# Kernel optimization log

Measured on AMD Instinct MI355X. Metric: run time of the kernel, lower is better.

## Reference

```python
import jax, jax.numpy as jnp
import numpy as np

N = 8192
TEMP = 0.5
EPS = 1e-12


def _normalize(z):
    # F.normalize(z, p=2, dim=1): x / max(||x||, eps)
    n = jnp.sqrt(jnp.sum(z * z, axis=1, keepdims=True))
    return z / jnp.maximum(n, EPS)


def _gcn(edge_index, edge_weight, x, w, b):
    # torch.sparse.mm(adj, x @ w): out[row] += adj[row, col] * support[col]
    support = x @ w
    msg = support[edge_index[1]] * edge_weight[:, None]
    return jax.ops.segment_sum(msg, edge_index[0], num_segments=N) + b


def _encoder(edge_index, edge_weight, feat, w_l1a, b_l1a, w_l1b, b_l1b, w_g1, b_g1, w_g2, b_g2):
    x = jax.nn.relu(feat @ w_l1a + b_l1a) @ w_l1b + b_l1b  # [N, 32]
    h = jax.nn.relu(_gcn(edge_index, edge_weight, x, w_g1, b_g1))  # [N, hid]
    return _gcn(edge_index, edge_weight, h, w_g2, b_g2)  # [N, act_fn]


def _proj(h, w_fc1, b_fc1, w_fc2, b_fc2):
    return jax.nn.elu(h @ w_fc1 + b_fc1) @ w_fc2 + b_fc2


def _loss(z1, z2):
    z1n = _normalize(z1)
    z2n = _normalize(z2)
    refl = jnp.exp((z1n @ z1n.T) / TEMP)      # [N, N]
    between = jnp.exp((z1n @ z2n.T) / TEMP)   # [N, N]
    denom = refl.sum(1) + between.sum(1) - jnp.diagonal(refl)
    return -jnp.log(jnp.diagonal(between) / denom)


def setup_inputs() -> dict:
    key = jax.random.key(0)
    ks = jax.random.split(key, 20)
    E = 262144
    in_dim, hid_dim, act_fn, out_dim = 512, 256, 128, 64

    def kaiming(k, shape):
        fan_in = shape[0]
        bound = np.sqrt(6.0 / fan_in)
        return jax.random.uniform(k, shape, jnp.float32, -bound, bound)

    return {
        "feat1": jax.random.normal(ks[0], (N, in_dim), jnp.float32),
        "feat2": jax.random.normal(ks[1], (N, in_dim), jnp.float32),
        "edge_index1": jax.random.randint(ks[2], (2, E), 0, N, jnp.int32),
        "edge_weight1": jax.random.uniform(ks[3], (E,), jnp.float32),
        "edge_index2": jax.random.randint(ks[4], (2, E), 0, N, jnp.int32),
        "edge_weight2": jax.random.uniform(ks[5], (E,), jnp.float32),
        "w_l1a": kaiming(ks[6], (in_dim, 64)),
        "b_l1a": jnp.zeros((64,), jnp.float32),
        "w_l1b": kaiming(ks[7], (64, 32)),
        "b_l1b": jnp.zeros((32,), jnp.float32),
        "w_g1": kaiming(ks[8], (32, hid_dim)),
        "b_g1": jnp.zeros((hid_dim,), jnp.float32),
        "w_g2": kaiming(ks[9], (hid_dim, act_fn)),
        "b_g2": jnp.zeros((act_fn,), jnp.float32),
        "w_fc1": kaiming(ks[10], (act_fn, out_dim)),
        "b_fc1": jnp.zeros((out_dim,), jnp.float32),
        "w_fc2": kaiming(ks[11], (out_dim, act_fn)),
        "b_fc2": jnp.zeros((act_fn,), jnp.float32),
    }


def reference(feat1, feat2, edge_index1, edge_weight1, edge_index2, edge_weight2,
              w_l1a, b_l1a, w_l1b, b_l1b, w_g1, b_g1, w_g2, b_g2,
              w_fc1, b_fc1, w_fc2, b_fc2):
    h1 = _encoder(edge_index1, edge_weight1, feat1, w_l1a, b_l1a, w_l1b, b_l1b, w_g1, b_g1, w_g2, b_g2)
    h2 = _encoder(edge_index2, edge_weight2, feat2, w_l1a, b_l1a, w_l1b, b_l1b, w_g1, b_g1, w_g2, b_g2)
    z1 = _proj(h1, w_fc1, b_fc1, w_fc2, b_fc2)
    z2 = _proj(h2, w_fc1, b_fc1, w_fc2, b_fc2)
    l1 = _loss(z1, z2)
    l2 = _loss(z2, z1)
    return ((l1 + l2) * 0.5).mean()
```

## Files before the change

### kernel.cpp

```cpp
#include <hip/hip_runtime.h>
#include <hip/hip_bf16.h>
#include <math.h>


#define NROWS 8192
#define MROWS 16384
#define NEDGE 262144

typedef __attribute__((ext_vector_type(8))) short bf16x8;
typedef __attribute__((ext_vector_type(4))) float f32x4;
typedef __attribute__((ext_vector_type(2))) float f32x2;
typedef long long i64;

__device__ __forceinline__ short f2bf(float f){
  union { float f; unsigned u; } cv; cv.f = f;
  unsigned u = cv.u;
  unsigned r = (u + 0x7fffu + ((u >> 16) & 1u)) >> 16;
  return (short)r;
}
__device__ __forceinline__ f32x4 mfma16(bf16x8 a, bf16x8 b, f32x4 c){
  return __builtin_amdgcn_mfma_f32_16x16x32_bf16(a, b, c, 0, 0, 0);
}
__device__ __forceinline__ float fexp2(float x){
#if __has_builtin(__builtin_amdgcn_exp2f)
  return __builtin_amdgcn_exp2f(x);
#else
  return exp2f(x);
#endif
}

__device__ unsigned char f2e4m3_sw(float f){
  float a = fabsf(f);
  unsigned s = (__float_as_uint(f)>>24)&0x80u;
  if (!(a>0.f)) return (unsigned char)s;
  if (a>448.f) a=448.f;
  int e; frexpf(a,&e);
  int eff=e-1;
  unsigned code;
  if (eff<-6){
    float q=rintf(a*512.f);
    code=(unsigned)q; if(code>7)code=7;
  } else {
    float q=rintf(a*exp2f((float)(3-eff)));
    unsigned mant=(unsigned)q;
    if(mant>=16){mant=8;eff++;}
    if(eff>8) return (unsigned char)(s|0x7e);
    code=((unsigned)(eff+7)<<3)|(mant-8);
  }
  return (unsigned char)(s|code);
}
__device__ __forceinline__ unsigned short pack2fp8(float a, float b){
#if __has_builtin(__builtin_amdgcn_cvt_pk_fp8_f32)
  int v = __builtin_amdgcn_cvt_pk_fp8_f32(a, b, 0, false);
  return (unsigned short)(v & 0xffff);
#else
  return (unsigned short)((unsigned)f2e4m3_sw(a) | ((unsigned)f2e4m3_sw(b)<<8));
#endif
}

struct WtArgs {
  const float* src[6];
  short* dst[6];
  int K[6], N[6];
  int off[7];
  int nwt;
};
__global__ void setup_k(WtArgs a, const int* __restrict__ ei1, const int* __restrict__ ei2,
                        int* __restrict__ deg1, int* __restrict__ deg2){
  int b = blockIdx.x;
  if (b < a.nwt){
    int i = b*256 + threadIdx.x;
    if (i >= a.off[6]) return;
    int s = 0;
    #pragma unroll
    for (int j=1;j<6;j++) if (i >= a.off[j]) s=j;
    int l = i - a.off[s];
    int K=a.K[s], N=a.N[s];
    int k=l/N, n=l-k*N;
    a.dst[s][(long)n*K+k] = f2bf(a.src[s][l]);
  } else {
    int hb = b - a.nwt;
    const int* ei = (hb < NEDGE/256) ? ei1 : ei2;
    int* deg = (hb < NEDGE/256) ? deg1 : deg2;
    int e = (hb % (NEDGE/256))*256 + threadIdx.x;
    atomicAdd(&deg[ei[e]], 1);
  }
}

__global__ __launch_bounds__(256) void mlp12_k(const float* __restrict__ F0, const float* __restrict__ F1,
                                               const short* __restrict__ Wa, const float* __restrict__ ba,
                                               const short* __restrict__ Wb, const float* __restrict__ bb,
                                               short* __restrict__ xb){
  __shared__ short As[32*520];
  __shared__ short a1s[32*72];
  const int tid = threadIdx.x;
  const int m0 = blockIdx.x*32;
  const float* F = (m0 < NROWS) ? (F0 + (long)m0*512) : (F1 + (long)(m0-NROWS)*512);
  {
    float4 st[16];
    #pragma unroll
    for (int i=0;i<16;i++) st[i] = *(const float4*)(F + (long)(i*256+tid)*4);
    #pragma unroll
    for (int i=0;i<16;i++){
      int idx = i*256+tid, row = idx>>7, c4 = idx&127;
      unsigned lo = (unsigned)(unsigned short)f2bf(st[i].x) | ((unsigned)(unsigned short)f2bf(st[i].y)<<16);
      unsigned hi = (unsigned)(unsigned short)f2bf(st[i].z) | ((unsigned)(unsigned short)f2bf(st[i].w)<<16);
      uint2 o = {lo, hi};
      *(uint2*)&As[row*520 + c4*4] = o;
    }
  }
  __syncthreads();
  const int wave = tid>>6, lane = tid&63, quad = lane>>4, cl = lane&15;
  f32x4 zero = {0.f,0.f,0.f,0.f};
  {
    const int wno = wave*16;
    f32x4 acc[2] = {zero, zero};
    #pragma unroll
    for (int kc=0;kc<16;kc++){
      const int ko = kc*32 + quad*8;
      bf16x8 a0 = *(const bf16x8*)&As[(cl)*520 + ko];
      bf16x8 a1 = *(const bf16x8*)&As[(16+cl)*520 + ko];
      bf16x8 b = *(const bf16x8*)(Wa + (long)(wno + cl)*512 + ko);
      acc[0] = mfma16(a0, b, acc[0]);
      acc[1] = mfma16(a1, b, acc[1]);
    }
    int col = wno + cl;
    float bv = ba[col];
    #pragma unroll
    for (int mt=0;mt<2;mt++)
      #pragma unroll
      for (int r=0;r<4;r++)
        a1s[(mt*16 + quad*4 + r)*72 + col] = f2bf(fmaxf(acc[mt][r] + bv, 0.f));
  }
  __syncthreads();
  if (wave < 2){
    f32x4 acc2[2] = {zero, zero};
    #pragma unroll
    for (int kc=0;kc<2;kc++){
      const int ko = kc*32 + quad*8;
      bf16x8 a = *(const bf16x8*)&a1s[(wave*16+cl)*72 + ko];
      #pragma unroll
      for (int nt=0;nt<2;nt++){
        bf16x8 b = *(const bf16x8*)(Wb + (long)(nt*16 + cl)*64 + ko);
        acc2[nt] = mfma16(a, b, acc2[nt]);
      }
    }
    #pragma unroll
    for (int nt=0;nt<2;nt++){
      int col = nt*16 + cl;
      float bv = bb[col];
      #pragma unroll
      for (int r=0;r<4;r++)
        xb[(long)(m0 + wave*16 + quad*4 + r)*32 + col] = f2bf(acc2[nt][r] + bv);
    }
  }
}

__global__ void scan2_k(const int* __restrict__ deg1, int* __restrict__ rs1, int* __restrict__ cur1,
                        const int* __restrict__ deg2, int* __restrict__ rs2, int* __restrict__ cur2){
  const int* deg = blockIdx.x ? deg2 : deg1;
  int* rowstart = blockIdx.x ? rs2 : rs1;
  int* cursor = blockIdx.x ? cur2 : cur1;
  __shared__ int csum[256];
  __shared__ int base[257];
  int t = threadIdx.x;
  int loc[32];
  int s = 0;
  for (int j=0;j<32;j++){ int d = deg[t*32+j]; loc[j] = s; s += d; }
  csum[t] = s;
  __syncthreads();
  if (t==0){ int a=0; for (int i=0;i<256;i++){ base[i]=a; a+=csum[i]; } base[256]=a; }
  __syncthreads();
  for (int j=0;j<32;j++){ int v = base[t] + loc[j]; rowstart[t*32+j]=v; cursor[t*32+j]=v; }
  if (t==0) rowstart[NROWS] = base[256];
}
__global__ void fill2_k(const int* __restrict__ ei1, const float* __restrict__ w1, int* __restrict__ cur1,
                        int* __restrict__ ecol1, float* __restrict__ ew1,
                        const int* __restrict__ ei2, const float* __restrict__ w2, int* __restrict__ cur2,
                        int* __restrict__ ecol2, float* __restrict__ ew2){
  int b = blockIdx.x;
  bool g2 = (b >= NEDGE/256);
  const int* ei = g2 ? ei2 : ei1;
  const float* w = g2 ? w2 : w1;
  int* cursor = g2 ? cur2 : cur1;
  int* ecol = g2 ? ecol2 : ecol1;
  float* ew = g2 ? ew2 : ew1;
  int e = (b % (NEDGE/256))*256 + threadIdx.x;
  int r = ei[e];
  int p = atomicAdd(&cursor[r], 1);
  ecol[p] = ei[NEDGE + e];
  ew[p] = w[e];
}

__device__ __forceinline__ void acc8(float* acc, int4 v, float f){
  const unsigned* u = (const unsigned*)&v;
  #pragma unroll
  for (int i=0;i<4;i++){
    union{unsigned x; float y;} lo, hi;
    lo.x = u[i] << 16;
    hi.x = u[i] & 0xffff0000u;
    acc[2*i]   = fmaf(f, lo.y, acc[2*i]);
    acc[2*i+1] = fmaf(f, hi.y, acc[2*i+1]);
  }
}
template<int C>
__device__ __forceinline__ void gather_row(float* acc, const short* sb,
                                           const int* ec, const float* w, int s, int e){
  int k = s;
  for (; k+16 <= e; k+=16){
    int c[16]; float f[16]; int4 v[16];
    #pragma unroll
    for (int u=0;u<16;u++){ c[u]=ec[k+u]; f[u]=w[k+u]; }
    #pragma unroll
    for (int u=0;u<16;u++) v[u] = *(const int4*)(sb + (long)c[u]*C);
    #pragma unroll
    for (int u=0;u<16;u++) acc8(acc, v[u], f[u]);
  }
  for (; k+4 <= e; k+=4){
    int c0=ec[k],c1=ec[k+1],c2=ec[k+2],c3=ec[k+3];
    float f0=w[k],f1=w[k+1],f2=w[k+2],f3=w[k+3];
    int4 v0 = *(const int4*)(sb + (long)c0*C);
    int4 v1 = *(const int4*)(sb + (long)c1*C);
    int4 v2 = *(const int4*)(sb + (long)c2*C);
    int4 v3 = *(const int4*)(sb + (long)c3*C);
    acc8(acc,v0,f0); acc8(acc,v1,f1); acc8(acc,v2,f2); acc8(acc,v3,f3);
  }
  for (; k < e; k++){
    int4 v0 = *(const int4*)(sb + (long)ec[k]*C);
    acc8(acc,v0,w[k]);
  }
}

template<int C, bool RELU, bool HASB>
__global__ __launch_bounds__(256) void gather_k(const short* __restrict__ sup,
    const int* __restrict__ rs1, const int* __restrict__ ec1, const float* __restrict__ w1,
    const int* __restrict__ rs2, const int* __restrict__ ec2, const float* __restrict__ w2,
    const float* __restrict__ bias, short* __restrict__ out){
  constexpr int G = C/8;
  const int g = threadIdx.x % G;
  const int sub = threadIdx.x / G;
  const int row = blockIdx.x*(256/G) + sub;
  const int* rs; const int* ec; const float* w; int soff, lr;
  if (row < NROWS){ rs=rs1; ec=ec1; w=w1; soff=0; lr=row; }
  else            { rs=rs2; ec=ec2; w=w2; soff=NROWS; lr=row-NROWS; }
  const short* sb = sup + (long)soff*C + g*8;
  float acc[8];
  #pragma unroll
  for (int j=0;j<8;j++) acc[j] = HASB ? bias[g*8+j] : 0.f;
  gather_row<C>(acc, sb, ec, w, rs[lr], rs[lr+1]);
  int4 ov;
  unsigned* ou = (unsigned*)&ov;
  #pragma unroll
  for (int i=0;i<4;i++){
    float a0 = acc[2*i], a1 = acc[2*i+1];
    if (RELU){ a0 = fmaxf(a0,0.f); a1 = fmaxf(a1,0.f); }
    ou[i] = (unsigned)(unsigned short)f2bf(a0) | ((unsigned)(unsigned short)f2bf(a1)<<16);
  }
  *(int4*)(out + (long)row*C + g*8) = ov;
}

__global__ __launch_bounds__(256) void gg_k(const short* __restrict__ xb,
    const int* __restrict__ rs1, const int* __restrict__ ec1, const float* __restrict__ w1,
    const int* __restrict__ rs2, const int* __restrict__ ec2, const float* __restrict__ w2,
    const short* __restrict__ Wg1, const float* __restrict__ bg1,
    const short* __restrict__ Wg2, short* __restrict__ s2){
  __shared__ short axs[64*40];
  __shared__ short hbs[64*264];
  const int tid = threadIdx.x;
  const int m0 = blockIdx.x*64;
  {
    const int g = tid & 3, sub = tid >> 2;
    const int row = m0 + sub;
    const int* rs; const int* ec; const float* w; int soff, lr;
    if (row < NROWS){ rs=rs1; ec=ec1; w=w1; soff=0; lr=row; }
    else            { rs=rs2; ec=ec2; w=w2; soff=NROWS; lr=row-NROWS; }
    const short* sb = xb + (long)soff*32 + g*8;
    float acc[8];
    #pragma unroll
    for (int j=0;j<8;j++) acc[j] = 0.f;
    gather_row<32>(acc, sb, ec, w, rs[lr], rs[lr+1]);
    int4 ov;
    unsigned* ou = (unsigned*)&ov;
    #pragma unroll
    for (int i=0;i<4;i++)
      ou[i] = (unsigned)(unsigned short)f2bf(acc[2*i]) | ((unsigned)(unsigned short)f2bf(acc[2*i+1])<<16);
    *(int4*)&axs[sub*40 + g*8] = ov;
  }
  __syncthreads();
  const int wave = tid>>6, lane = tid&63, quad = lane>>4, cl = lane&15;
  f32x4 zero = {0.f,0.f,0.f,0.f};
  {
    const int wno = wave*64;
    f32x4 acc[4][4];
    #pragma unroll
    for (int i=0;i<4;i++)
      #pragma unroll
      for (int j=0;j<4;j++) acc[i][j]=zero;
    const int ko = quad*8;
    bf16x8 a[4], b[4];
    #pragma unroll
    for (int mt=0;mt<4;mt++)
      a[mt] = *(const bf16x8*)&axs[(mt*16+cl)*40 + ko];
    #pragma unroll
    for (int nt=0;nt<4;nt++)
      b[nt] = *(const bf16x8*)(Wg1 + (long)(wno + nt*16 + cl)*32 + ko);
    #pragma unroll
    for (int mt=0;mt<4;mt++)
      #pragma unroll
      for (int nt=0;nt<4;nt++)
        acc[mt][nt] = mfma16(a[mt], b[nt], acc[mt][nt]);
    #pragma unroll
    for (int nt=0;nt<4;nt++){
      int col = wno + nt*16 + cl;
      float bv = bg1[col];
      #pragma unroll
      for (int mt=0;mt<4;mt++)
        #pragma unroll
        for (int r=0;r<4;r++)
          hbs[(mt*16 + quad*4 + r)*264 + col] = f2bf(fmaxf(acc[mt][nt][r] + bv, 0.f));
    }
  }
  __syncthreads();
  {
    const int wno = wave*32;
    f32x4 acc[4][2];
    #pragma unroll
    for (int i=0;i<4;i++){ acc[i][0]=zero; acc[i][1]=zero; }
    #pragma unroll
    for (int kc=0;kc<8;kc++){
      const int ko = kc*32 + quad*8;
      bf16x8 a[4], b[2];
      #pragma unroll
      for (int mt=0;mt<4;mt++)
        a[mt] = *(const bf16x8*)&hbs[(mt*16+cl)*264 + ko];
      #pragma unroll
      for (int nt=0;nt<2;nt++)
        b[nt] = *(const bf16x8*)(Wg2 + (long)(wno + nt*16 + cl)*256 + ko);
      #pragma unroll
      for (int mt=0;mt<4;mt++)
        #pragma unroll
        for (int nt=0;nt<2;nt++)
          acc[mt][nt] = mfma16(a[mt], b[nt], acc[mt][nt]);
    }
    #pragma unroll
    for (int mt=0;mt<4;mt++)
      #pragma unroll
      for (int nt=0;nt<2;nt++){
        int col = wno + nt*16 + cl;
        #pragma unroll
        for (int r=0;r<4;r++)
          s2[(long)(m0 + mt*16 + quad*4 + r)*128 + col] = f2bf(acc[mt][nt][r]);
      }
  }
}

__global__ __launch_bounds__(256) void pn_k(const short* __restrict__ hh,
    const short* __restrict__ Wf1, const float* __restrict__ bf1,
    const short* __restrict__ Wf2, const float* __restrict__ bf2,
    unsigned short* __restrict__ Zf, float* __restrict__ bdot){
  __shared__ short hs[64*136];
  __shared__ short t2s[64*72];
  __shared__ float zs[64*132];
  __shared__ float sp[4][64];
  __shared__ float dp[4][32];
  __shared__ float rnS[64];
  const float SQKE = 1.6986436f;
  const int tid = threadIdx.x;
  const int wave = tid>>6, lane = tid&63, quad = lane>>4, cl = lane&15;
  const int m0h = blockIdx.x*32;
  {
    const short* r1 = hh + (long)m0h*128;
    const short* r2 = hh + (long)(NROWS + m0h)*128;
    #pragma unroll
    for (int i=0;i<2;i++){
      int idx = i*256 + tid;
      int row = idx >> 4, c16 = idx & 15;
      *(int4*)&hs[row*136 + c16*8] = *(const int4*)(r1 + row*128 + c16*8);
      *(int4*)&hs[(32+row)*136 + c16*8] = *(const int4*)(r2 + row*128 + c16*8);
    }
  }
  __syncthreads();
  f32x4 zero = {0.f,0.f,0.f,0.f};
  {
    const int wno = wave*16;
    f32x4 acc[4];
    #pragma unroll
    for (int i=0;i<4;i++) acc[i]=zero;
    #pragma unroll
    for (int kc=0;kc<4;kc++){
      const int ko = kc*32 + quad*8;
      bf16x8 a[4], b;
      #pragma unroll
      for (int mt=0;mt<4;mt++)
        a[mt] = *(const bf16x8*)&hs[(mt*16+cl)*136 + ko];
      b = *(const bf16x8*)(Wf1 + (long)(wno + cl)*128 + ko);
      #pragma unroll
      for (int mt=0;mt<4;mt++) acc[mt] = mfma16(a[mt], b, acc[mt]);
    }
    int col = wno + cl;
    float bv = bf1[col];
    #pragma unroll
    for (int mt=0;mt<4;mt++)
      #pragma unroll
      for (int r=0;r<4;r++){
        float v = acc[mt][r] + bv;
        v = (v > 0.f) ? v : expm1f(v);
        t2s[(mt*16 + quad*4 + r)*72 + col] = f2bf(v);
      }
  }
  __syncthreads();
  {
    const int wno = wave*32;
    f32x4 acc[4][2];
    #pragma unroll
    for (int i=0;i<4;i++){ acc[i][0]=zero; acc[i][1]=zero; }
    #pragma unroll
    for (int kc=0;kc<2;kc++){
      const int ko = kc*32 + quad*8;
      bf16x8 a[4], b[2];
      #pragma unroll
      for (int mt=0;mt<4;mt++)
        a[mt] = *(const bf16x8*)&t2s[(mt*16+cl)*72 + ko];
      #pragma unroll
      for (int nt=0;nt<2;nt++)
        b[nt] = *(const bf16x8*)(Wf2 + (long)(wno + nt*16 + cl)*64 + ko);
      #pragma unroll
      for (int mt=0;mt<4;mt++)
        #pragma unroll
        for (int nt=0;nt<2;nt++)
          acc[mt][nt] = mfma16(a[mt], b[nt], acc[mt][nt]);
    }
    #pragma unroll
    for (int mt=0;mt<4;mt++)
      #pragma unroll
      for (int nt=0;nt<2;nt++){
        int col = wno + nt*16 + cl;
        float bv = bf2[col];
        #pragma unroll
        for (int r=0;r<4;r++)
          zs[(mt*16 + quad*4 + r)*132 + col] = acc[mt][nt][r] + bv;
      }
  }
  __syncthreads();
  {
    int row = tid & 63, qtr = tid >> 6;
    const float* zr = &zs[row*132 + qtr*32];
    float s = 0.f;
    #pragma unroll 8
    for (int c=0;c<32;c++) s += zr[c]*zr[c];
    sp[qtr][row] = s;
    if (row < 32){
      const float* zb_ = &zs[(row+32)*132 + qtr*32];
      float d = 0.f;
      #pragma unroll 8
      for (int c=0;c<32;c++) d += zr[c]*zb_[c];
      dp[qtr][row] = d;
    }
  }
  __syncthreads();
  if (tid < 64){
    float ssq = sp[0][tid]+sp[1][tid]+sp[2][tid]+sp[3][tid];
    rnS[tid] = 1.f / fmaxf(sqrtf(ssq), 1e-12f);
  }
  __syncthreads();
  if (tid < 32){
    float dot = dp[0][tid]+dp[1][tid]+dp[2][tid]+dp[3][tid];
    bdot[m0h + tid] = dot * rnS[tid] * rnS[tid+32];
  }
  {
    int lr = tid >> 2;
    int grow = (lr < 32) ? (m0h + lr) : (NROWS + m0h + lr - 32);
    float s = rnS[lr] * SQKE;
    int p0 = (tid & 3)*16;
    #pragma unroll
    for (int pp=0;pp<16;pp++){
      int p = p0 + pp;
      int d = p>>1, h = p&1, kc = d>>3, q = (d>>1)&3, j4 = d&1;
      long o = ((long)(grow>>4)*512 + kc*128 + j4 + ((grow&15)+16*q)*2)*2 + h;
      Zf[o] = pack2fp8(zs[lr*132 + 2*p]*s, zs[lr*132 + 2*p + 1]*s);
    }
  }
}

__global__ __launch_bounds__(256,4) void gram3_k(const unsigned char* __restrict__ Zf,
                                                 float* __restrict__ P){
  __shared__ float srow[4][64];
  __shared__ float scol[4][64];
  const int wave = threadIdx.x>>6, lane = threadIdx.x&63;
  const int t = blockIdx.x*4 + wave;
  int ti = (int)((513.0f - sqrtf(513.0f*513.0f - 8.0f*(float)t))*0.5f);
  while ((ti+1)*256 - ((ti+1)*ti)/2 <= t) ti++;
  while (ti*256 - (ti*(ti-1))/2 > t) ti--;
  const int tj = ti + (t - (ti*256 - (ti*(ti-1))/2));
  const unsigned char* za = Zf + (long)ti*16*512 + lane*8;
  const unsigned char* zb = Zf + (long)tj*16*512 + lane*8;

  f32x4 zero = {0.f,0.f,0.f,0.f};
  f32x4 acc[4][4];
  #pragma unroll
  for (int i=0;i<4;i++)
    #pragma unroll
    for (int j=0;j<4;j++) acc[i][j]=zero;

  i64 aA[4], bA[4], aB[4], bB[4];
  #pragma unroll
  for (int x=0;x<4;x++){
    aA[x] = *(const i64*)(za + (x*4+0)*512);
    bA[x] = *(const i64*)(zb + (x*4+0)*512);
  }
  #pragma unroll
  for (int kc=0;kc<4;kc++){
    i64* ac = (kc&1) ? aB : aA;
    i64* bc = (kc&1) ? bB : bA;
    i64* an = (kc&1) ? aA : aB;
    i64* bn = (kc&1) ? bA : bB;
    if (kc<3){
      #pragma unroll
      for (int x=0;x<4;x++){
        an[x] = *(const i64*)(za + (x*4+kc+1)*512);
        bn[x] = *(const i64*)(zb + (x*4+kc+1)*512);
      }
    }
    #pragma unroll
    for (int mt=0;mt<4;mt++)
      #pragma unroll
      for (int nt=0;nt<4;nt++)
        acc[mt][nt] = __builtin_amdgcn_mfma_f32_16x16x32_fp8_fp8(ac[mt], bc[nt], acc[mt][nt], 0, 0, 0);
  }

  const int quad = lane>>4, cl = lane&15;
  f32x2 z2 = {0.f,0.f};
  f32x2 rs01[4] = {z2,z2,z2,z2}, rs23[4] = {z2,z2,z2,z2};
  f32x2 cs[4] = {z2,z2,z2,z2};
  #pragma unroll
  for (int mt=0;mt<4;mt++){
    #pragma unroll
    for (int nt=0;nt<4;nt++){
      f32x4 v = acc[mt][nt];
      float e0 = fexp2(v[0]), e1 = fexp2(v[1]);
      float e2 = fexp2(v[2]), e3 = fexp2(v[3]);
      f32x2 p01 = {e0,e1}, p23 = {e2,e3};
      rs01[mt] += p01; rs23[mt] += p23;
      cs[nt] += p01; cs[nt] += p23;
    }
  }
  #pragma unroll
  for (int mt=0;mt<4;mt++){
    union{f32x2 v; double d;} u0, u1;
    u0.v = rs01[mt]; u1.v = rs23[mt];
    #pragma unroll
    for (int m=1;m<16;m<<=1){
      union{double d; f32x2 v;} o0, o1;
      o0.d = __shfl_xor(u0.d, m); o1.d = __shfl_xor(u1.d, m);
      u0.v += o0.v; u1.v += o1.v;
    }
    if (cl==0){
      f32x4 rv = {u0.v.x, u0.v.y, u1.v.x, u1.v.y};
      *(f32x4*)&srow[wave][mt*16 + quad*4] = rv;
    }
  }
  __threadfence_block();
  P[((long)ti*256 + tj)*64 + lane] = srow[wave][lane];
  if (ti != tj){
    #pragma unroll
    for (int nt=0;nt<4;nt++){
      float s = cs[nt].x + cs[nt].y;
      s += __shfl_xor(s,16); s += __shfl_xor(s,32);
      if (quad==0) scol[wave][nt*16 + cl] = s;
    }
    __threadfence_block();
    P[((long)tj*256 + ti)*64 + lane] = scol[wave][lane];
  }
}

__global__ void rloss_k(const float* __restrict__ P, const float* __restrict__ bdot,
                        float* __restrict__ out){
  __shared__ float red[256];
  const float E2 = 7.3890560989306495f;
  int t = threadIdx.x;
  int i = blockIdx.x*256 + t;
  int j = i + NROWS;
  const float* p1 = P + (long)(i>>6)*256*64 + (i&63);
  const float* p2 = P + (long)(j>>6)*256*64 + (j&63);
  float s1 = 0.f, s2 = 0.f;
  #pragma unroll 8
  for (int b=0;b<256;b++){ s1 += p1[b*64]; s2 += p2[b*64]; }
  float lb = 2.f * bdot[i];
  float term = 0.5f * ((logf(s1 - E2) - lb) + (logf(s2 - E2) - lb));
  red[t]=term; __syncthreads();
  for (int st=128; st>0; st>>=1){ if (t<st) red[t]+=red[t+st]; __syncthreads(); }
  if (t==0) atomicAdd(out, red[0] / (float)NROWS);
}

extern "C" void kernel_launch(void* const* d_in, const int* in_sizes, int n_in,
                              void* d_out, int out_size, void* d_ws, size_t ws_size,
                              hipStream_t stream){
  const float* feat1 = (const float*)d_in[0];
  const float* feat2 = (const float*)d_in[1];
  const int*   ei1   = (const int*)d_in[2];
  const float* w1    = (const float*)d_in[3];
  const int*   ei2   = (const int*)d_in[4];
  const float* w2    = (const float*)d_in[5];
  const float* w_l1a = (const float*)d_in[6];
  const float* b_l1a = (const float*)d_in[7];
  const float* w_l1b = (const float*)d_in[8];
  const float* b_l1b = (const float*)d_in[9];
  const float* w_g1  = (const float*)d_in[10];
  const float* b_g1  = (const float*)d_in[11];
  const float* w_g2  = (const float*)d_in[12];
  const float* b_g2  = (const float*)d_in[13];
  const float* w_fc1 = (const float*)d_in[14];
  const float* b_fc1 = (const float*)d_in[15];
  const float* w_fc2 = (const float*)d_in[16];
  const float* b_fc2 = (const float*)d_in[17];

  float* P = (float*)d_ws;
  char* base = (char*)d_ws;
  size_t off = (size_t)17<<20;
  auto alloc = [&](size_t bytes)->void*{
    void* r = base + off;
    off = (off + bytes + 255) & ~(size_t)255;
    return r;
  };
  short* xb   = (short*)alloc((size_t)MROWS*32*2);
  short* s2   = (short*)alloc((size_t)MROWS*128*2);
  short* hh   = (short*)alloc((size_t)MROWS*128*2);
  short* wl1a_t = (short*)alloc(512*64*2);
  short* wl1b_t = (short*)alloc(64*32*2);
  short* wg1_t  = (short*)alloc(32*256*2);
  short* wg2_t  = (short*)alloc(256*128*2);
  short* wfc1_t = (short*)alloc(128*64*2);
  short* wfc2_t = (short*)alloc(64*128*2);
  unsigned short* Zf = (unsigned short*)alloc((size_t)MROWS*128);
  int*   deg1 = (int*)alloc(NROWS*4);
  int*   deg2 = (int*)alloc(NROWS*4);
  int* rs1  = (int*)alloc((NROWS+1)*4);
  int* cur1 = (int*)alloc(NROWS*4);
  int* rs2  = (int*)alloc((NROWS+1)*4);
  int* cur2 = (int*)alloc(NROWS*4);
  int*   ecol1 = (int*)alloc((size_t)NEDGE*4);
  float* ewt1  = (float*)alloc((size_t)NEDGE*4);
  int*   ecol2 = (int*)alloc((size_t)NEDGE*4);
  float* ewt2  = (float*)alloc((size_t)NEDGE*4);
  float* bdot  = (float*)alloc(NROWS*4);

  hipMemsetAsync(deg1, 0, (size_t)2*NROWS*4, stream);
  hipMemsetAsync(d_out, 0, sizeof(float), stream);

  WtArgs wa;
  wa.src[0]=w_l1a; wa.dst[0]=wl1a_t; wa.K[0]=512; wa.N[0]=64;
  wa.src[1]=w_l1b; wa.dst[1]=wl1b_t; wa.K[1]=64;  wa.N[1]=32;
  wa.src[2]=w_g1;  wa.dst[2]=wg1_t;  wa.K[2]=32;  wa.N[2]=256;
  wa.src[3]=w_g2;  wa.dst[3]=wg2_t;  wa.K[3]=256; wa.N[3]=128;
  wa.src[4]=w_fc1; wa.dst[4]=wfc1_t; wa.K[4]=128; wa.N[4]=64;
  wa.src[5]=w_fc2; wa.dst[5]=wfc2_t; wa.K[5]=64;  wa.N[5]=128;
  wa.off[0]=0;
  for (int i=0;i<6;i++) wa.off[i+1] = wa.off[i] + wa.K[i]*wa.N[i];
  wa.nwt = (wa.off[6]+255)/256;

  setup_k<<<wa.nwt + 2*(NEDGE/256),256,0,stream>>>(wa, ei1, ei2, deg1, deg2);
  scan2_k<<<2,256,0,stream>>>(deg1, rs1, cur1, deg2, rs2, cur2);
  fill2_k<<<2*(NEDGE/256),256,0,stream>>>(ei1, w1, cur1, ecol1, ewt1,
                                          ei2, w2, cur2, ecol2, ewt2);

  mlp12_k<<<MROWS/32,256,0,stream>>>(feat1, feat2, wl1a_t, b_l1a, wl1b_t, b_l1b, xb);
  gg_k<<<MROWS/64,256,0,stream>>>(xb, rs1,ecol1,ewt1, rs2,ecol2,ewt2,
                                  wg1_t, b_g1, wg2_t, s2);
  gather_k<128,false,true><<<MROWS/16,256,0,stream>>>(s2, rs1,ecol1,ewt1,
                                                      rs2,ecol2,ewt2, b_g2, hh);
  pn_k<<<NROWS/32,256,0,stream>>>(hh, wfc1_t, b_fc1, wfc2_t, b_fc2, Zf, bdot);

  gram3_k<<<8224,256,0,stream>>>((const unsigned char*)Zf, P);
  rloss_k<<<NROWS/256,256,0,stream>>>(P, bdot, (float*)d_out);
}
```

Measured before the change: 269.3 us.

## Overlap exp epilogue with MFMA row tiles in gram kernel; parallel scan

The gram kernel now keeps all B fragments in registers and computes one 16-row tile at a time, double-buffering A loads and doing the exp and row reduction of the previous tile while the MFMAs for the current tile run. This is meant to hide transcendental and shuffle latency behind matrix work and to cut peak accumulator register pressure. Separately, the CSR scan kernel replaces its serial single-thread prefix over 256 partial sums with a Hillis-Steele shared-memory scan. The scan change is small, and the restructured gram loop could change register allocation or how the compiler schedules instructions.

```diff
diff --git a/kernel.cpp b/kernel.cpp
--- a/kernel.cpp
+++ b/kernel.cpp
@@ -162,17 +162,23 @@
   int* rowstart = blockIdx.x ? rs2 : rs1;
   int* cursor = blockIdx.x ? cur2 : cur1;
   __shared__ int csum[256];
-  __shared__ int base[257];
   int t = threadIdx.x;
   int loc[32];
   int s = 0;
   for (int j=0;j<32;j++){ int d = deg[t*32+j]; loc[j] = s; s += d; }
-  csum[t] = s;
-  __syncthreads();
-  if (t==0){ int a=0; for (int i=0;i<256;i++){ base[i]=a; a+=csum[i]; } base[256]=a; }
-  __syncthreads();
-  for (int j=0;j<32;j++){ int v = base[t] + loc[j]; rowstart[t*32+j]=v; cursor[t*32+j]=v; }
-  if (t==0) rowstart[NROWS] = base[256];
+  int v = s;
+  csum[t] = v;
+  __syncthreads();
+  for (int st=1; st<256; st<<=1){
+    int o = (t >= st) ? csum[t-st] : 0;
+    __syncthreads();
+    v += o;
+    csum[t] = v;
+    __syncthreads();
+  }
+  int base = v - s;
+  for (int j=0;j<32;j++){ int w = base + loc[j]; rowstart[t*32+j]=w; cursor[t*32+j]=w; }
+  if (t==255) rowstart[NROWS] = v;
 }
 __global__ void fill2_k(const int* __restrict__ ei1, const float* __restrict__ w1, int* __restrict__ cur1,
                         int* __restrict__ ecol1, float* __restrict__ ew1,
@@ -494,60 +500,38 @@
   const int tj = ti + (t - (ti*256 - (ti*(ti-1))/2));
   const unsigned char* za = Zf + (long)ti*16*512 + lane*8;
   const unsigned char* zb = Zf + (long)tj*16*512 + lane*8;
+  const int quad = lane>>4, cl = lane&15;
 
   f32x4 zero = {0.f,0.f,0.f,0.f};
-  f32x4 acc[4][4];
-  #pragma unroll
-  for (int i=0;i<4;i++)
-    #pragma unroll
-    for (int j=0;j<4;j++) acc[i][j]=zero;
-
-  i64 aA[4], bA[4], aB[4], bB[4];
-  #pragma unroll
-  for (int x=0;x<4;x++){
-    aA[x] = *(const i64*)(za + (x*4+0)*512);
-    bA[x] = *(const i64*)(zb + (x*4+0)*512);
-  }
-  #pragma unroll
-  for (int kc=0;kc<4;kc++){
-    i64* ac = (kc&1) ? aB : aA;
-    i64* bc = (kc&1) ? bB : bA;
-    i64* an = (kc&1) ? aA : aB;
-    i64* bn = (kc&1) ? bA : bB;
-    if (kc<3){
-      #pragma unroll
-      for (int x=0;x<4;x++){
-        an[x] = *(const i64*)(za + (x*4+kc+1)*512);
-        bn[x] = *(const i64*)(zb + (x*4+kc+1)*512);
-      }
-    }
-    #pragma unroll
-    for (int mt=0;mt<4;mt++)
-      #pragma unroll
-      for (int nt=0;nt<4;nt++)
-        acc[mt][nt] = __builtin_amdgcn_mfma_f32_16x16x32_fp8_fp8(ac[mt], bc[nt], acc[mt][nt], 0, 0, 0);
-  }
-
-  const int quad = lane>>4, cl = lane&15;
   f32x2 z2 = {0.f,0.f};
-  f32x2 rs01[4] = {z2,z2,z2,z2}, rs23[4] = {z2,z2,z2,z2};
   f32x2 cs[4] = {z2,z2,z2,z2};
-  #pragma unroll
-  for (int mt=0;mt<4;mt++){
+
+  i64 Bf[4][4];
+  #pragma unroll
+  for (int nt=0;nt<4;nt++)
+    #pragma unroll
+    for (int kc=0;kc<4;kc++)
+      Bf[nt][kc] = *(const i64*)(zb + (nt*4+kc)*512);
+
+  i64 Ab[2][4];
+  #pragma unroll
+  for (int kc=0;kc<4;kc++) Ab[0][kc] = *(const i64*)(za + kc*512);
+  #pragma unroll
+  for (int kc=0;kc<4;kc++) Ab[1][kc] = *(const i64*)(za + (4+kc)*512);
+
+  auto exprow = [&](const f32x4* ar, int mt){
+    f32x2 r01 = z2, r23 = z2;
     #pragma unroll
     for (int nt=0;nt<4;nt++){
-      f32x4 v = acc[mt][nt];
+      f32x4 v = ar[nt];
       float e0 = fexp2(v[0]), e1 = fexp2(v[1]);
       float e2 = fexp2(v[2]), e3 = fexp2(v[3]);
       f32x2 p01 = {e0,e1}, p23 = {e2,e3};
-      rs01[mt] += p01; rs23[mt] += p23;
+      r01 += p01; r23 += p23;
       cs[nt] += p01; cs[nt] += p23;
     }
-  }
-  #pragma unroll
-  for (int mt=0;mt<4;mt++){
     union{f32x2 v; double d;} u0, u1;
-    u0.v = rs01[mt]; u1.v = rs23[mt];
+    u0.v = r01; u1.v = r23;
     #pragma unroll
     for (int m=1;m<16;m<<=1){
       union{double d; f32x2 v;} o0, o1;
@@ -558,7 +542,36 @@
       f32x4 rv = {u0.v.x, u0.v.y, u1.v.x, u1.v.y};
       *(f32x4*)&srow[wave][mt*16 + quad*4] = rv;
     }
-  }
+  };
+
+  f32x4 acc2[2][4];
+  #pragma unroll
+  for (int nt=0;nt<4;nt++){
+    f32x4 a = zero;
+    #pragma unroll
+    for (int kc=0;kc<4;kc++)
+      a = __builtin_amdgcn_mfma_f32_16x16x32_fp8_fp8(Ab[0][kc], Bf[nt][kc], a, 0, 0, 0);
+    acc2[0][nt] = a;
+  }
+  #pragma unroll
+  for (int mt=1; mt<4; mt++){
+    const int cur = mt&1, prv = cur^1;
+    if (mt<3){
+      #pragma unroll
+      for (int kc=0;kc<4;kc++) Ab[prv][kc] = *(const i64*)(za + ((mt+1)*4+kc)*512);
+    }
+    #pragma unroll
+    for (int nt=0;nt<4;nt++){
+      f32x4 a = zero;
+      #pragma unroll
+      for (int kc=0;kc<4;kc++)
+        a = __builtin_amdgcn_mfma_f32_16x16x32_fp8_fp8(Ab[cur][kc], Bf[nt][kc], a, 0, 0, 0);
+      acc2[cur][nt] = a;
+    }
+    exprow(&acc2[prv][0], mt-1);
+  }
+  exprow(&acc2[1][0], 3);
+
   __threadfence_block();
   P[((long)ti*256 + tj)*64 + lane] = srow[wave][lane];
   if (ti != tj){
```

Result: faster. 263.8 us (-2.0%).
